# Kernel tuning notes

Measured on AMD Instinct MI355X. Metric: run time of the kernel, lower is better.

Reference implementation:

```python
import jax, jax.numpy as jnp
import numpy as np

B, S, D, H = 4, 2048, 2048, 16
DH = D // H  # 128
BASE = 10000.0


def _rope_tables(seq_len, d_head, dtype):
    # inv_freq over even indices of half-dim, freqs duplicated (cat(freqs, freqs))
    inv_freq = 1.0 / (BASE ** (jnp.arange(0, d_head, 2, dtype=jnp.float32) / d_head))
    t = jnp.arange(seq_len, dtype=jnp.float32)
    freqs = jnp.einsum('i,j->ij', t, inv_freq)          # [S, d_head/2]
    emb = jnp.concatenate([freqs, freqs], axis=-1)       # [S, d_head]
    return jnp.cos(emb).astype(dtype), jnp.sin(emb).astype(dtype)


def _rotate_half(x):
    x1, x2 = jnp.split(x, 2, axis=-1)
    return jnp.concatenate([-x2, x1], axis=-1)


def setup_inputs() -> dict:
    key = jax.random.key(0)
    k1, k2, k3 = jax.random.split(key, 3)
    x = jax.random.normal(k1, (B, S, D), dtype=jnp.float32)
    Wqkv = jax.random.normal(k2, (3 * D, D), dtype=jnp.float32) * (D ** -0.5)
    Wo = jax.random.normal(k3, (D, D), dtype=jnp.float32) * (D ** -0.5)
    return {"x": x, "Wqkv": Wqkv, "Wo": Wo}


def reference(x, Wqkv, Wo) -> jnp.ndarray:
    b, s, d = x.shape
    # fused QKV projection: Linear(d, 3d, bias=False) -> x @ Wqkv.T
    qkv = jnp.einsum('bsd,ed->bse', x, Wqkv)                      # [B,S,3D]
    qkv = qkv.reshape(b, s, 3, H, DH)                              # (n n_head d_head)
    q = jnp.transpose(qkv[:, :, 0], (0, 2, 1, 3))                  # [B,H,S,DH]
    k = jnp.transpose(qkv[:, :, 1], (0, 2, 1, 3))
    v = jnp.transpose(qkv[:, :, 2], (0, 2, 1, 3))
    # rotary position embedding
    cos, sin = _rope_tables(s, DH, x.dtype)                        # [S,DH]
    cos = cos[None, None, :, :]
    sin = sin[None, None, :, :]
    q = q * cos + _rotate_half(q) * sin
    k = k * cos + _rotate_half(k) * sin
    # eval-path manual causal attention
    scale = 1.0 / jnp.sqrt(jnp.asarray(DH, dtype=x.dtype))
    scores = jnp.einsum('bhqd,bhkd->bhqk', q, k) * scale           # [B,H,S,S]
    causal = jnp.tril(jnp.ones((s, s), dtype=bool))
    scores = jnp.where(causal[None, None, :, :], scores, -jnp.inf)
    pattern = jax.nn.softmax(scores, axis=-1)
    z = jnp.einsum('bhqk,bhkd->bhqd', pattern, v)                  # [B,H,S,DH]
    z = jnp.transpose(z, (0, 2, 1, 3)).reshape(b, s, d)            # [B,S,D]
    return jnp.einsum('bsd,ed->bse', z, Wo)
```

## Files before the change

### kernel.cpp

```cpp
#include <hip/hip_runtime.h>
#include <hip/hip_bf16.h>
#include <stdint.h>

#define B_ 4
#define S_ 2048
#define D_ 2048
#define H_ 16
#define DH_ 128

typedef short bf8_t __attribute__((ext_vector_type(8)));
typedef float f4_t  __attribute__((ext_vector_type(4)));

__device__ __forceinline__ unsigned short f2bf(float f) {
  __hip_bfloat16 h = __float2bfloat16(f);
  return *reinterpret_cast<const unsigned short*>(&h);
}
__device__ __forceinline__ float bf2f(unsigned short u) {
  return __uint_as_float(((unsigned int)u) << 16);
}

__device__ __forceinline__ void gload_lds16(const void* g, void* lds) {
  __builtin_amdgcn_global_load_lds(
      (const __attribute__((address_space(1))) unsigned int*)(uintptr_t)g,
      (__attribute__((address_space(3))) unsigned int*)(unsigned int)(uintptr_t)lds,
      16, 0, 0);
}

__global__ __launch_bounds__(256) void conv_all(
    const float* __restrict__ x, const float* __restrict__ wqkv,
    const float* __restrict__ wo, unsigned short* __restrict__ xb,
    unsigned short* __restrict__ wqkvb, unsigned short* __restrict__ wob) {
  int b = blockIdx.x;
  const float* in;
  unsigned short* out;
  int i;
  if (b < 16384)      { in = x;    out = xb;    i = b * 256 + threadIdx.x; }
  else if (b < 28672) { in = wqkv; out = wqkvb; i = (b - 16384) * 256 + threadIdx.x; }
  else                { in = wo;   out = wob;   i = (b - 28672) * 256 + threadIdx.x; }
  float4 v = ((const float4*)in)[i];
  ushort4 u;
  u.x = f2bf(v.x); u.y = f2bf(v.y); u.z = f2bf(v.z); u.w = f2bf(v.w);
  ((ushort4*)out)[i] = u;
}

template <int EPI>
__global__ __launch_bounds__(512, 2) void gemm256(
    const unsigned short* __restrict__ A, const unsigned short* __restrict__ Bt,
    float* __restrict__ Cf, unsigned short* __restrict__ Cb,
    int M, int N, int K) {
  __shared__ unsigned short AB[2][2][8192];
  const int tid  = threadIdx.x;
  const int lane = tid & 63;
  const int wv   = tid >> 6;
  const int wr   = wv >> 2;
  const int wc   = wv & 3;
  const int rsel = lane & 15;
  const int g    = lane >> 4;
  const int qr0  = g * 4;

  int id  = blockIdx.y * gridDim.x + blockIdx.x;
  int cpx = (gridDim.x * gridDim.y) >> 3;
  int swz = (id & 7) * cpx + (id >> 3);
  const int bm = (swz / gridDim.x) * 256;
  const int bn = (swz % gridDim.x) * 256;

  const int NS = K >> 5;

  const int ob0 = tid * 16, ob1 = ob0 + 8192;
  const int row0 = ob0 >> 6, row1 = ob1 >> 6;
  const int g0 = ((ob0 >> 4) & 3) ^ ((row0 >> 1) & 3);
  const int g1 = ((ob1 >> 4) & 3) ^ ((row1 >> 1) & 3);
  const unsigned short* Ag0 = A + (size_t)(bm + row0) * K + g0 * 8;
  const unsigned short* Ag1 = A + (size_t)(bm + row1) * K + g1 * 8;
  const unsigned short* Bg0 = Bt + (size_t)(bn + row0) * K + g0 * 8;
  const unsigned short* Bg1 = Bt + (size_t)(bn + row1) * K + g1 * 8;

  f4_t acc[8][4];
#pragma unroll
  for (int i = 0; i < 8; ++i)
#pragma unroll
    for (int j = 0; j < 4; ++j) acc[i][j] = (f4_t){0.f, 0.f, 0.f, 0.f};

  int aoff[8], boff[4];
#pragma unroll
  for (int i = 0; i < 8; ++i) {
    int arow = wr * 128 + i * 16 + rsel;
    aoff[i] = arow * 64 + ((g * 16) ^ ((arow & 6) << 3));
  }
#pragma unroll
  for (int j = 0; j < 4; ++j) {
    int brow = wc * 64 + j * 16 + rsel;
    boff[j] = brow * 64 + ((g * 16) ^ ((brow & 6) << 3));
  }

#define STAGE(sl)                                                        \
  {                                                                      \
    int slot_ = (sl) & 1;                                                \
    int ks_   = (sl) << 5;                                               \
    gload_lds16(Ag0 + ks_, (char*)&AB[slot_][0][0] + ob0);               \
    gload_lds16(Ag1 + ks_, (char*)&AB[slot_][0][0] + ob1);               \
    gload_lds16(Bg0 + ks_, (char*)&AB[slot_][1][0] + ob0);               \
    gload_lds16(Bg1 + ks_, (char*)&AB[slot_][1][0] + ob1);               \
  }

  STAGE(0); STAGE(1);

  for (int s = 0; s < NS; ++s) {
    if (s + 1 < NS) asm volatile("s_waitcnt vmcnt(4)" ::: "memory");
    else            asm volatile("s_waitcnt vmcnt(0)" ::: "memory");
    __builtin_amdgcn_s_barrier();
    asm volatile("" ::: "memory");

    const char* As_ = (const char*)&AB[s & 1][0][0];
    const char* Bs_ = (const char*)&AB[s & 1][1][0];
    bf8_t af[8], bfr[4];
#pragma unroll
    for (int i = 0; i < 8; ++i) af[i] = *(const bf8_t*)(As_ + aoff[i]);
#pragma unroll
    for (int j = 0; j < 4; ++j) bfr[j] = *(const bf8_t*)(Bs_ + boff[j]);

    asm volatile("s_waitcnt lgkmcnt(0)" ::: "memory");
    __builtin_amdgcn_s_barrier();
    asm volatile("" ::: "memory");
    if (s + 2 < NS) STAGE(s + 2);

    __builtin_amdgcn_s_setprio(1);
#pragma unroll
    for (int i = 0; i < 8; ++i)
#pragma unroll
      for (int j = 0; j < 4; ++j)
        acc[i][j] = __builtin_amdgcn_mfma_f32_16x16x32_bf16(af[i], bfr[j], acc[i][j], 0, 0, 0);
    __builtin_amdgcn_s_setprio(0);
  }
#undef STAGE

#pragma unroll
  for (int i = 0; i < 8; ++i) {
#pragma unroll
    for (int j = 0; j < 4; ++j) {
#pragma unroll
      for (int r = 0; r < 4; ++r) {
        int row = bm + wr * 128 + i * 16 + qr0 + r;
        int col = bn + wc * 64 + j * 16 + rsel;
        float v = acc[i][j][r];
        if (EPI == 0) {
          Cf[(size_t)row * N + col] = v;
        } else {
          int c = col >> 11, h = (col >> 7) & (H_ - 1), dh = col & (DH_ - 1);
          int b = row >> 11, s = row & (S_ - 1);
          size_t dst = ((((size_t)c * B_ + b) * H_ + h) * S_ + s) * DH_ + dh;
          Cb[dst] = f2bf(v);
        }
      }
    }
  }
}

__global__ void rope_tab(float* __restrict__ tc, float* __restrict__ ts) {
  int s = blockIdx.x;
  int i = threadIdx.x;
  float inv = powf(10000.0f, -(float)i / 64.0f);
  float f   = (float)s * inv;
  tc[s * 64 + i] = cosf(f);
  ts[s * 64 + i] = sinf(f);
}

__global__ __launch_bounds__(256) void rope_k(
    unsigned short* __restrict__ Kk,
    const float* __restrict__ tc, const float* __restrict__ ts) {
  int idx = blockIdx.x * 256 + threadIdx.x;
  int iv  = idx & 7;
  int s   = (idx >> 3) & (S_ - 1);
  int bh  = idx >> 14;
  size_t base = ((size_t)bh * S_ + s) * DH_;
  int i0 = iv * 8;
  bf8_t x1 = *(const bf8_t*)&Kk[base + i0];
  bf8_t x2 = *(const bf8_t*)&Kk[base + i0 + 64];
  const float* tcp = tc + s * 64 + i0;
  const float* tsp = ts + s * 64 + i0;
  bf8_t y1, y2;
#pragma unroll
  for (int e = 0; e < 8; ++e) {
    float c = tcp[e], sn = tsp[e];
    float a = bf2f((unsigned short)x1[e]);
    float b = bf2f((unsigned short)x2[e]);
    y1[e] = (short)f2bf(a * c - b * sn);
    y2[e] = (short)f2bf(b * c + a * sn);
  }
  *(bf8_t*)&Kk[base + i0]      = y1;
  *(bf8_t*)&Kk[base + i0 + 64] = y2;
}

__global__ __launch_bounds__(512) void attn_fwd(
    const unsigned short* __restrict__ Q, const unsigned short* __restrict__ Kk,
    const unsigned short* __restrict__ V, unsigned short* __restrict__ Z,
    const float* __restrict__ tabc, const float* __restrict__ tabs) {
  __shared__ unsigned short Ks[3][64 * 128];
  __shared__ unsigned short Vt[2][128 * 64];
  __shared__ unsigned short Pw[8][32 * 64];
  const int tid  = threadIdx.x;
  const int lane = tid & 63;
  const int wv   = tid >> 6;

  int id  = blockIdx.y * gridDim.x + blockIdx.x;
  int x   = id & 7;
  int idx = id >> 3;
  const int bh = x * 8 + (idx & 7);
  const int q0 = (7 - (idx >> 3)) * 256;

  const size_t base = (size_t)bh * S_ * DH_;
  const int rsel = lane & 15;
  const int g    = lane >> 4;
  const int kof  = g * 8;
  const int qr0  = g * 4;
  const int qlo  = q0 + wv * 32;
  const int qhi  = qlo + 31;
  const float sl2 = 0.08838834764831845f * 1.4426950408889634f;

  bf8_t aq[2][4];
#pragma unroll
  for (int rg = 0; rg < 2; ++rg) {
    const int qrow = qlo + rg * 16 + rsel;
#pragma unroll
    for (int kc = 0; kc < 4; ++kc)
      aq[rg][kc] = *(const bf8_t*)&Q[base + (size_t)qrow * DH_ + kc * 32 + kof];
    const float* tcr = tabc + (size_t)qrow * 64;
    const float* tsr = tabs + (size_t)qrow * 64;
#pragma unroll
    for (int kc = 0; kc < 2; ++kc)
#pragma unroll
      for (int e = 0; e < 8; ++e) {
        int i = kc * 32 + kof + e;
        float c  = tcr[i], sn = tsr[i];
        float x1 = bf2f((unsigned short)aq[rg][kc][e]);
        float x2 = bf2f((unsigned short)aq[rg][kc + 2][e]);
        aq[rg][kc][e]     = (short)f2bf((x1 * c - x2 * sn) * sl2);
        aq[rg][kc + 2][e] = (short)f2bf((x2 * c + x1 * sn) * sl2);
      }
  }

  bf8_t vones;
#pragma unroll
  for (int e = 0; e < 8; ++e) vones[e] = (short)0x3F80;

  f4_t o[2][9];
#pragma unroll
  for (int rg = 0; rg < 2; ++rg)
#pragma unroll
    for (int nf = 0; nf < 9; ++nf) o[rg][nf] = (f4_t){0.f, 0.f, 0.f, 0.f};
  float mrow[2][4] = {{-3e30f, -3e30f, -3e30f, -3e30f},
                      {-3e30f, -3e30f, -3e30f, -3e30f}};
  const int nt = q0 / 64 + 4;

  const int kvp = tid & 31;
  const int vc0 = (tid >> 5) * 8;

#define KSTAGE(tt)                                                            \
  {                                                                           \
    const unsigned short* gK_ = Kk + base + (size_t)(tt) * 64 * DH_;          \
    int slot_ = (tt) % 3;                                                     \
    _Pragma("unroll")                                                         \
    for (int c = 0; c < 2; ++c) {                                             \
      int ob = (c * 512 + tid) * 16;                                          \
      int row = ob >> 8;                                                      \
      int scol = (ob & 255) ^ ((row & 7) << 4);                               \
      gload_lds16(gK_ + (size_t)row * DH_ + (scol >> 1),                      \
                  (char*)&Ks[slot_][0] + ob);                                 \
    }                                                                         \
  }
#define VTWRITE(buf_)                                                         \
  {                                                                           \
    unsigned int* Vt32 = (unsigned int*)&Vt[buf_][0];                         \
    _Pragma("unroll")                                                         \
    for (int e = 0; e < 8; ++e) {                                             \
      unsigned int val = (unsigned short)vlo[e] |                             \
                         ((unsigned int)(unsigned short)vhi[e] << 16);        \
      Vt32[(vc0 + e) * 32 + (kvp ^ (e << 2))] = val;                          \
    }                                                                         \
  }

  bf8_t vlo, vhi;
  vlo = *(const bf8_t*)&V[base + (size_t)(2 * kvp) * DH_ + vc0];
  vhi = *(const bf8_t*)&V[base + (size_t)(2 * kvp + 1) * DH_ + vc0];
  KSTAGE(0);
  KSTAGE(1);
  VTWRITE(0);

  for (int t = 0; t < nt; ++t) {
    const int curV = t & 1;
    const int curK = t % 3;
    const bool pfV = (t + 1 < nt);
    const bool pfK = (t + 2 < nt);

    if (pfV) asm volatile("s_waitcnt vmcnt(2)" ::: "memory");
    else     asm volatile("s_waitcnt vmcnt(0)" ::: "memory");
    asm volatile("s_waitcnt lgkmcnt(0)" ::: "memory");
    __builtin_amdgcn_s_barrier();
    asm volatile("" ::: "memory");

    if (pfV) {
      const unsigned short* gV = V + base + (size_t)(t + 1) * 64 * DH_;
      vlo = *(const bf8_t*)&gV[(size_t)(2 * kvp) * DH_ + vc0];
      vhi = *(const bf8_t*)&gV[(size_t)(2 * kvp + 1) * DH_ + vc0];
    }
    if (pfK) KSTAGE(t + 2);

    const int kv0 = t * 64;
    const bool active = (kv0 <= qhi);
    const bool domask = active && (kv0 + 63 > qlo);

    if (active) {
      f4_t sacc[2][4];
#pragma unroll
      for (int rg = 0; rg < 2; ++rg)
#pragma unroll
        for (int cf = 0; cf < 4; ++cf) sacc[rg][cf] = (f4_t){0.f, 0.f, 0.f, 0.f};
      __builtin_amdgcn_s_setprio(1);
#pragma unroll
      for (int cf = 0; cf < 4; ++cf)
#pragma unroll
        for (int kc = 0; kc < 4; ++kc) {
          int krow = cf * 16 + rsel;
          bf8_t bk = *(const bf8_t*)&Ks[curK][krow * 128 + ((kc * 32 + kof) ^ ((krow & 7) << 3))];
          sacc[0][cf] = __builtin_amdgcn_mfma_f32_16x16x32_bf16(aq[0][kc], bk, sacc[0][cf], 0, 0, 0);
          sacc[1][cf] = __builtin_amdgcn_mfma_f32_16x16x32_bf16(aq[1][kc], bk, sacc[1][cf], 0, 0, 0);
        }
      __builtin_amdgcn_s_setprio(0);

      if (domask) {
#pragma unroll
        for (int rg = 0; rg < 2; ++rg)
#pragma unroll
          for (int cf = 0; cf < 4; ++cf) {
            int kvabs = kv0 + cf * 16 + rsel;
#pragma unroll
            for (int r = 0; r < 4; ++r) {
              int qabs = qlo + rg * 16 + qr0 + r;
              if (kvabs > qabs) sacc[rg][cf][r] = -3e30f;
            }
          }
      }

      float tmr[2][4];
      bool needr = false;
#pragma unroll
      for (int rg = 0; rg < 2; ++rg)
#pragma unroll
        for (int r = 0; r < 4; ++r) {
          tmr[rg][r] = fmaxf(fmaxf(sacc[rg][0][r], sacc[rg][1][r]),
                             fmaxf(sacc[rg][2][r], sacc[rg][3][r]));
          needr = needr || (tmr[rg][r] > mrow[rg][r] + 11.f);
        }
      if (__any(needr)) {
#pragma unroll
        for (int rg = 0; rg < 2; ++rg)
#pragma unroll
          for (int r = 0; r < 4; ++r) {
            float m = tmr[rg][r];
#pragma unroll
            for (int d = 1; d < 16; d <<= 1) m = fmaxf(m, __shfl_xor(m, d, 16));
            float nm = fmaxf(mrow[rg][r], m);
            float sc = exp2f(mrow[rg][r] - nm);
            mrow[rg][r] = nm;
#pragma unroll
            for (int nf = 0; nf < 9; ++nf) o[rg][nf][r] *= sc;
          }
      }
#pragma unroll
      for (int rg = 0; rg < 2; ++rg)
#pragma unroll
        for (int cf = 0; cf < 4; ++cf)
#pragma unroll
          for (int r = 0; r < 4; ++r)
            sacc[rg][cf][r] = exp2f(sacc[rg][cf][r] - mrow[rg][r]);

      unsigned short* P = &Pw[wv][0];
#pragma unroll
      for (int rg = 0; rg < 2; ++rg)
#pragma unroll
        for (int cf = 0; cf < 4; ++cf)
#pragma unroll
          for (int r = 0; r < 4; ++r) {
            int prow = rg * 16 + qr0 + r;
            P[prow * 64 + ((cf * 16 + rsel) ^ (((prow >> 1) & 7) << 3))] = f2bf(sacc[rg][cf][r]);
          }
    }

    if (pfV) VTWRITE(curV ^ 1);

    if (active) {
      unsigned short* P = &Pw[wv][0];
      __builtin_amdgcn_s_setprio(1);
#pragma unroll
      for (int kc2 = 0; kc2 < 2; ++kc2) {
        bf8_t pa0, pa1;
        {
          int pr0 = rsel;
          int pr1 = 16 + rsel;
          pa0 = *(const bf8_t*)&P[pr0 * 64 + ((kc2 * 32 + kof) ^ (((pr0 >> 1) & 7) << 3))];
          pa1 = *(const bf8_t*)&P[pr1 * 64 + ((kc2 * 32 + kof) ^ (((pr1 >> 1) & 7) << 3))];
        }
#pragma unroll
        for (int nf = 0; nf < 8; ++nf) {
          int vrow = nf * 16 + rsel;
          bf8_t bv = *(const bf8_t*)&Vt[curV][vrow * 64 + ((kc2 * 32 + kof) ^ ((vrow & 7) << 3))];
          o[0][nf] = __builtin_amdgcn_mfma_f32_16x16x32_bf16(pa0, bv, o[0][nf], 0, 0, 0);
          o[1][nf] = __builtin_amdgcn_mfma_f32_16x16x32_bf16(pa1, bv, o[1][nf], 0, 0, 0);
        }
        o[0][8] = __builtin_amdgcn_mfma_f32_16x16x32_bf16(pa0, vones, o[0][8], 0, 0, 0);
        o[1][8] = __builtin_amdgcn_mfma_f32_16x16x32_bf16(pa1, vones, o[1][8], 0, 0, 0);
      }
      __builtin_amdgcn_s_setprio(0);
    }
  }
#undef KSTAGE
#undef VTWRITE

  const int b = bh >> 4, h = bh & 15;
#pragma unroll
  for (int rg = 0; rg < 2; ++rg)
#pragma unroll
    for (int r = 0; r < 4; ++r) {
      float inv = 1.0f / o[rg][8][r];
      int s = qlo + rg * 16 + qr0 + r;
      size_t rowo = ((size_t)b * S_ + s) * D_ + h * DH_;
#pragma unroll
      for (int nf = 0; nf < 8; ++nf)
        Z[rowo + nf * 16 + rsel] = f2bf(o[rg][nf][r] * inv);
    }
}

extern "C" void kernel_launch(void* const* d_in, const int* in_sizes, int n_in,
                              void* d_out, int out_size, void* d_ws, size_t ws_size,
                              hipStream_t stream) {
  const float* x    = (const float*)d_in[0];
  const float* Wqkv = (const float*)d_in[1];
  const float* Wo   = (const float*)d_in[2];
  float* out = (float*)d_out;

  const size_t QKV_ELEMS = (size_t)B_ * H_ * S_ * DH_;
  char* w = (char*)d_ws;
  unsigned short* xb = (unsigned short*)w;
  unsigned short* z  = xb;
  w += (size_t)8192 * 2048 * 2;
  unsigned short* wqkvb = (unsigned short*)w; w += (size_t)6144 * 2048 * 2;
  unsigned short* wob   = (unsigned short*)w; w += (size_t)2048 * 2048 * 2;
  unsigned short* qq = (unsigned short*)w;    w += QKV_ELEMS * 2;
  unsigned short* kk = (unsigned short*)w;    w += QKV_ELEMS * 2;
  unsigned short* vv = (unsigned short*)w;    w += QKV_ELEMS * 2;
  float* tabc = (float*)w; w += (size_t)S_ * 64 * 4;
  float* tabs = (float*)w; w += (size_t)S_ * 64 * 4;
  if ((size_t)(w - (char*)d_ws) > ws_size) return;

  conv_all<<<32768, 256, 0, stream>>>(x, Wqkv, Wo, xb, wqkvb, wob);
  gemm256<1><<<dim3(24, 32), 512, 0, stream>>>(xb, wqkvb, nullptr, qq, 8192, 6144, 2048);
  rope_tab<<<2048, 64, 0, stream>>>(tabc, tabs);
  rope_k<<<4096, 256, 0, stream>>>(kk, tabc, tabs);
  attn_fwd<<<dim3(S_ / 256, B_ * H_), 512, 0, stream>>>(qq, kk, vv, z, tabc, tabs);
  gemm256<0><<<dim3(8, 32), 512, 0, stream>>>(z, wob, out, nullptr, 8192, 2048, 2048);
}
```

Before: 429.7 us.

## Deepen GEMM LDS pipeline to four stages with split-phase MFMA scheduling

Expands the GEMM shared-memory ring from two to four slots and prefetches three K-steps ahead. The output projection removes the second barrier per iteration. The QKV projection splits the B fragment reads and MFMAs into two barrier-separated phases to interleave LDS reads with compute. The aim is to hide global-load latency and reduce sync stalls, at the cost of doubled LDS usage and extra barriers in the QKV variant.

```diff
diff --git a/kernel.cpp b/kernel.cpp
--- a/kernel.cpp
+++ b/kernel.cpp
@@ -43,12 +43,12 @@
   ((ushort4*)out)[i] = u;
 }
 
-template <int EPI>
+template <int EPI, int PIPE>
 __global__ __launch_bounds__(512, 2) void gemm256(
     const unsigned short* __restrict__ A, const unsigned short* __restrict__ Bt,
     float* __restrict__ Cf, unsigned short* __restrict__ Cb,
     int M, int N, int K) {
-  __shared__ unsigned short AB[2][2][8192];
+  __shared__ unsigned short AB[4][2][8192];
   const int tid  = threadIdx.x;
   const int lane = tid & 63;
   const int wv   = tid >> 6;
@@ -95,7 +95,7 @@
 
 #define STAGE(sl)                                                        \
   {                                                                      \
-    int slot_ = (sl) & 1;                                                \
+    int slot_ = (sl) & 3;                                                \
     int ks_   = (sl) << 5;                                               \
     gload_lds16(Ag0 + ks_, (char*)&AB[slot_][0][0] + ob0);               \
     gload_lds16(Ag1 + ks_, (char*)&AB[slot_][0][0] + ob1);               \
@@ -103,34 +103,78 @@
     gload_lds16(Bg1 + ks_, (char*)&AB[slot_][1][0] + ob1);               \
   }
 
-  STAGE(0); STAGE(1);
-
-  for (int s = 0; s < NS; ++s) {
-    if (s + 1 < NS) asm volatile("s_waitcnt vmcnt(4)" ::: "memory");
-    else            asm volatile("s_waitcnt vmcnt(0)" ::: "memory");
+  STAGE(0); STAGE(1); STAGE(2);
+
+  if (PIPE == 0) {
+    for (int s = 0; s < NS; ++s) {
+      if (s < NS - 2)       asm volatile("s_waitcnt vmcnt(8)" ::: "memory");
+      else if (s == NS - 2) asm volatile("s_waitcnt vmcnt(4)" ::: "memory");
+      else                  asm volatile("s_waitcnt vmcnt(0)" ::: "memory");
+      __builtin_amdgcn_s_barrier();
+      asm volatile("" ::: "memory");
+
+      const char* As_ = (const char*)&AB[s & 3][0][0];
+      const char* Bs_ = (const char*)&AB[s & 3][1][0];
+      bf8_t af[8], bfr[4];
+#pragma unroll
+      for (int i = 0; i < 8; ++i) af[i] = *(const bf8_t*)(As_ + aoff[i]);
+#pragma unroll
+      for (int j = 0; j < 4; ++j) bfr[j] = *(const bf8_t*)(Bs_ + boff[j]);
+
+      if (s + 3 < NS) STAGE(s + 3);
+
+      __builtin_amdgcn_s_setprio(1);
+#pragma unroll
+      for (int i = 0; i < 8; ++i)
+#pragma unroll
+        for (int j = 0; j < 4; ++j)
+          acc[i][j] = __builtin_amdgcn_mfma_f32_16x16x32_bf16(af[i], bfr[j], acc[i][j], 0, 0, 0);
+      __builtin_amdgcn_s_setprio(0);
+    }
+  } else {
+    asm volatile("s_waitcnt vmcnt(8)" ::: "memory");
     __builtin_amdgcn_s_barrier();
     asm volatile("" ::: "memory");
 
-    const char* As_ = (const char*)&AB[s & 1][0][0];
-    const char* Bs_ = (const char*)&AB[s & 1][1][0];
-    bf8_t af[8], bfr[4];
-#pragma unroll
-    for (int i = 0; i < 8; ++i) af[i] = *(const bf8_t*)(As_ + aoff[i]);
-#pragma unroll
-    for (int j = 0; j < 4; ++j) bfr[j] = *(const bf8_t*)(Bs_ + boff[j]);
-
-    asm volatile("s_waitcnt lgkmcnt(0)" ::: "memory");
-    __builtin_amdgcn_s_barrier();
-    asm volatile("" ::: "memory");
-    if (s + 2 < NS) STAGE(s + 2);
-
-    __builtin_amdgcn_s_setprio(1);
-#pragma unroll
-    for (int i = 0; i < 8; ++i)
-#pragma unroll
-      for (int j = 0; j < 4; ++j)
-        acc[i][j] = __builtin_amdgcn_mfma_f32_16x16x32_bf16(af[i], bfr[j], acc[i][j], 0, 0, 0);
-    __builtin_amdgcn_s_setprio(0);
+    for (int s = 0; s < NS; ++s) {
+      const char* As_ = (const char*)&AB[s & 3][0][0];
+      const char* Bs_ = (const char*)&AB[s & 3][1][0];
+      bf8_t af[8], bfr[4];
+
+#pragma unroll
+      for (int i = 0; i < 8; ++i) af[i] = *(const bf8_t*)(As_ + aoff[i]);
+      bfr[0] = *(const bf8_t*)(Bs_ + boff[0]);
+      bfr[1] = *(const bf8_t*)(Bs_ + boff[1]);
+      if (s + 3 < NS) STAGE(s + 3);
+      __builtin_amdgcn_s_barrier();
+      asm volatile("" ::: "memory");
+      __builtin_amdgcn_s_setprio(1);
+#pragma unroll
+      for (int i = 0; i < 8; ++i) {
+        acc[i][0] = __builtin_amdgcn_mfma_f32_16x16x32_bf16(af[i], bfr[0], acc[i][0], 0, 0, 0);
+        acc[i][1] = __builtin_amdgcn_mfma_f32_16x16x32_bf16(af[i], bfr[1], acc[i][1], 0, 0, 0);
+      }
+      __builtin_amdgcn_s_setprio(0);
+      __builtin_amdgcn_s_barrier();
+      asm volatile("" ::: "memory");
+
+      bfr[2] = *(const bf8_t*)(Bs_ + boff[2]);
+      bfr[3] = *(const bf8_t*)(Bs_ + boff[3]);
+      __builtin_amdgcn_s_barrier();
+      asm volatile("" ::: "memory");
+      __builtin_amdgcn_s_setprio(1);
+#pragma unroll
+      for (int i = 0; i < 8; ++i) {
+        acc[i][2] = __builtin_amdgcn_mfma_f32_16x16x32_bf16(af[i], bfr[2], acc[i][2], 0, 0, 0);
+        acc[i][3] = __builtin_amdgcn_mfma_f32_16x16x32_bf16(af[i], bfr[3], acc[i][3], 0, 0, 0);
+      }
+      __builtin_amdgcn_s_setprio(0);
+      if (s <= NS - 4)      asm volatile("s_waitcnt vmcnt(8)" ::: "memory");
+      else if (s == NS - 3) asm volatile("s_waitcnt vmcnt(4)" ::: "memory");
+      else                  asm volatile("s_waitcnt vmcnt(0)" ::: "memory");
+      __builtin_amdgcn_s_barrier();
+      asm volatile("" ::: "memory");
+    }
   }
 #undef STAGE
 
@@ -453,9 +497,9 @@
   if ((size_t)(w - (char*)d_ws) > ws_size) return;
 
   conv_all<<<32768, 256, 0, stream>>>(x, Wqkv, Wo, xb, wqkvb, wob);
-  gemm256<1><<<dim3(24, 32), 512, 0, stream>>>(xb, wqkvb, nullptr, qq, 8192, 6144, 2048);
+  gemm256<1, 1><<<dim3(24, 32), 512, 0, stream>>>(xb, wqkvb, nullptr, qq, 8192, 6144, 2048);
   rope_tab<<<2048, 64, 0, stream>>>(tabc, tabs);
   rope_k<<<4096, 256, 0, stream>>>(kk, tabc, tabs);
   attn_fwd<<<dim3(S_ / 256, B_ * H_), 512, 0, stream>>>(qq, kk, vv, z, tabc, tabs);
-  gemm256<0><<<dim3(8, 32), 512, 0, stream>>>(z, wob, out, nullptr, 8192, 2048, 2048);
-}
+  gemm256<0, 0><<<dim3(8, 32), 512, 0, stream>>>(z, wob, out, nullptr, 8192, 2048, 2048);
+}
```

After: 418.0 us. 2.7% less time.
